# Kernel optimization log

Hardware: AMD Instinct MI355X
Metric: run time of the kernel (lower is better)

The kernel has to match this reference:

```python
import jax, jax.numpy as jnp
import numpy as np

STRIDE = 1
PADDING = (1, 1, 1, 1)  # (left, right, top, bottom), as in torch F.pad for last two dims
NEG_INF = -jnp.inf


def maxplus_conv2d(x, kernel, stride=STRIDE):
    """Tropical (max-plus) conv2d, groups=1.
    x: [B, C, H, W] (already padded), kernel: [O, C, kh, kw].
    out[b,o,h,w] = max_{c,ki,kj} x[b,c,h*s+ki,w*s+kj] + kernel[o,c,ki,kj]
    """
    B, C, H, W = x.shape
    O, Cg, kh, kw = kernel.shape
    Ho = (H - kh) // stride + 1
    Wo = (W - kw) // stride + 1
    out = jnp.full((B, O, Ho, Wo), NEG_INF, dtype=x.dtype)
    # Loop over the small, fixed kernel taps (kh*kw = 9); reductions over the
    # channel axis stay fully vectorized and fuse into a single add+reduce-max.
    for ki in range(kh):
        for kj in range(kw):
            xs = x[:, :, ki:ki + Ho * stride:stride, kj:kj + Wo * stride:stride]  # [B,C,Ho,Wo]
            cand = jnp.max(xs[:, None, :, :, :] + kernel[None, :, :, ki, kj][:, :, :, None, None], axis=2)
            out = jnp.maximum(out, cand)
    return out


def setup_inputs() -> dict:
    key = jax.random.key(0)
    kx, kk = jax.random.split(key)
    x = jax.random.normal(kx, (8, 64, 64, 64), dtype=jnp.float32)
    kernel = jax.random.normal(kk, (64, 64, 3, 3), dtype=jnp.float32) * 0.1
    return {"x": x, "kernel": kernel}


def reference(x, kernel):
    left, right, top, bottom = PADDING
    # MaxPlus semifield: pad with the additive identity of max, i.e. -inf
    xp = jnp.pad(x, ((0, 0), (0, 0), (top, bottom), (left, right)), mode="constant", constant_values=NEG_INF)
    return maxplus_conv2d(xp, kernel, STRIDE)
```

## Files before the change

### kernel.cpp

```cpp
#include <hip/hip_runtime.h>

typedef float v2f __attribute__((ext_vector_type(2)));

#define NEG_INF (-__builtin_huge_valf())

#define CCH   4
#define HB    4
#define ROWS  (HB + 2)
#define XSTR  64
#define SLOTS 6

__device__ __forceinline__ float dpp_shr1(float v, float old) {
    return __int_as_float(__builtin_amdgcn_update_dpp(
        __float_as_int(old), __float_as_int(v), 0x111, 0xF, 0xF, false));
}
__device__ __forceinline__ float dpp_shl1(float v, float old) {
    return __int_as_float(__builtin_amdgcn_update_dpp(
        __float_as_int(old), __float_as_int(v), 0x101, 0xF, 0xF, false));
}

__global__ __launch_bounds__(64, 4)
void maxplus_conv2d_kernel(const float* __restrict__ x,
                           const float* __restrict__ kern,
                           float* __restrict__ out) {
    __shared__ float xs[CCH * ROWS * XSTR];

    const int tid = threadIdx.x;
    const int wg  = tid & 15;
    const int hr  = tid >> 4;
    const int w0  = wg << 2;

    const int h_base = blockIdx.x * HB;
    const int b      = blockIdx.y;
    const int o_base = blockIdx.z << 1;

    const float* xb = x + (size_t)b * 64 * 64 * 64;
    const float* gsrc[SLOTS];
    float*       xdst[SLOTS];
    bool         vmask[SLOTS];
#pragma unroll
    for (int k = 0; k < SLOTS; ++k) {
        int rowid = k * 4 + hr;
        int cl    = rowid / ROWS;
        int r     = rowid - cl * ROWS;
        int gh    = h_base + r - 1;
        bool valid = (unsigned)gh < 64u;
        int  ghc   = valid ? gh : 0;
        gsrc[k]  = xb + ((size_t)cl * 64 + ghc) * 64 + wg * 4;
        xdst[k]  = &xs[rowid * XSTR + wg * 4];
        vmask[k] = valid;
    }

    const float ninf = NEG_INF;

    float acc[2][4];
#pragma unroll
    for (int oo = 0; oo < 2; ++oo)
#pragma unroll
        for (int wi = 0; wi < 4; ++wi)
            acc[oo][wi] = NEG_INF;

    float4 R[SLOTS];
#pragma unroll
    for (int k = 0; k < SLOTS; ++k) R[k] = *(const float4*)gsrc[k];

#pragma unroll 1
    for (int cc = 0; cc < 64; cc += CCH) {
        __syncthreads();

#pragma unroll
        for (int k = 0; k < SLOTS; ++k) {
            float4 v = R[k];
            if (!vmask[k]) v = make_float4(NEG_INF, NEG_INF, NEG_INF, NEG_INF);
            *(float4*)xdst[k] = v;
        }

        __syncthreads();

        if (cc + CCH < 64) {
#pragma unroll
            for (int k = 0; k < SLOTS; ++k) {
                gsrc[k] += CCH * 64 * 64;
                R[k] = *(const float4*)gsrc[k];
            }
        }

        float kv[CCH][2][9];
#pragma unroll
        for (int cl = 0; cl < CCH; ++cl)
#pragma unroll
            for (int oo = 0; oo < 2; ++oo) {
                const float* kp = kern + ((size_t)(o_base + oo) * 64 + (cc + cl)) * 9;
#pragma unroll
                for (int t = 0; t < 9; ++t) kv[cl][oo][t] = kp[t];
            }

#pragma unroll
        for (int cl = 0; cl < CCH; ++cl) {
#pragma unroll
            for (int r = 0; r < 3; ++r) {
                const int rowid = cl * ROWS + hr + r;
                float4 m = *(const float4*)(&xs[rowid * XSTR + w0]);
                float le = dpp_shr1(m.w, ninf);
                float re = dpp_shl1(m.x, ninf);

                v2f P0 = {le,  m.x};
                v2f P1 = {m.y, m.z};
                v2f P2 = {m.w, re };
                v2f Q0 = {m.x, m.y};
                v2f Q1 = {m.z, m.w};

#pragma unroll
                for (int oo = 0; oo < 2; ++oo) {
                    const float* k9 = kv[cl][oo];
                    v2f ka = {k9[3*r+0], k9[3*r+0]};
                    v2f kb = {k9[3*r+1], k9[3*r+1]};
                    v2f kc = {k9[3*r+2], k9[3*r+2]};
                    v2f a0 = P0 + ka, b0 = P1 + ka;
                    v2f a1 = Q0 + kb, b1 = Q1 + kb;
                    v2f a2 = P1 + kc, b2 = P2 + kc;

                    acc[oo][0] = fmaxf(acc[oo][0], fmaxf(fmaxf(a0.x, a1.x), a2.x));
                    acc[oo][1] = fmaxf(acc[oo][1], fmaxf(fmaxf(a0.y, a1.y), a2.y));
                    acc[oo][2] = fmaxf(acc[oo][2], fmaxf(fmaxf(b0.x, b1.x), b2.x));
                    acc[oo][3] = fmaxf(acc[oo][3], fmaxf(fmaxf(b0.y, b1.y), b2.y));
                }
            }
        }
    }

    const int h = h_base + hr;
#pragma unroll
    for (int oo = 0; oo < 2; ++oo) {
        float4 v = make_float4(acc[oo][0], acc[oo][1], acc[oo][2], acc[oo][3]);
        *(float4*)(out + ((((size_t)b * 64 + (o_base + oo)) * 64 + h) * 64 + w0)) = v;
    }
}

extern "C" void kernel_launch(void* const* d_in, const int* in_sizes, int n_in,
                              void* d_out, int out_size, void* d_ws, size_t ws_size,
                              hipStream_t stream) {
    const float* x    = (const float*)d_in[0];
    const float* kern = (const float*)d_in[1];
    float* out = (float*)d_out;

    dim3 grid(16, 8, 32);
    dim3 block(64);
    maxplus_conv2d_kernel<<<grid, block, 0, stream>>>(x, kern, out);
}
```

Baseline: 110.6 us.

## Split channel reduction across two blocks, drop LDS staging, add max-merge pass

Removes the shared-memory staging and barriers. Each thread now loads its three input rows straight from global memory with register double-buffering of the next channel's rows and weights, and out-of-range rows point at a constant -inf row. When workspace is large enough, the 64-channel reduction is split into two halves across twice as many blocks, writing partial maxima to the output and the workspace. A second small kernel then merges the two with elementwise max. This adds parallelism and removes sync overhead, at the cost of an extra launch, extra global traffic, and less cross-thread reuse of input rows.

```diff
diff --git a/kernel.cpp b/kernel.cpp
--- a/kernel.cpp
+++ b/kernel.cpp
@@ -1,14 +1,12 @@
 #include <hip/hip_runtime.h>
-
-typedef float v2f __attribute__((ext_vector_type(2)));
 
 #define NEG_INF (-__builtin_huge_valf())
 
-#define CCH   4
-#define HB    4
-#define ROWS  (HB + 2)
-#define XSTR  64
-#define SLOTS 6
+#define N8 NEG_INF,NEG_INF,NEG_INF,NEG_INF,NEG_INF,NEG_INF,NEG_INF,NEG_INF
+__constant__ __align__(16) float NINF_ROW[64] = {N8,N8,N8,N8,N8,N8,N8,N8};
+#undef N8
+
+typedef float v2f __attribute__((ext_vector_type(2)));
 
 __device__ __forceinline__ float dpp_shr1(float v, float old) {
     return __int_as_float(__builtin_amdgcn_update_dpp(
@@ -22,33 +20,30 @@
 __global__ __launch_bounds__(64, 4)
 void maxplus_conv2d_kernel(const float* __restrict__ x,
                            const float* __restrict__ kern,
-                           float* __restrict__ out) {
-    __shared__ float xs[CCH * ROWS * XSTR];
-
+                           float* __restrict__ out0,
+                           float* __restrict__ out1,
+                           int c_count) {
     const int tid = threadIdx.x;
     const int wg  = tid & 15;
     const int hr  = tid >> 4;
     const int w0  = wg << 2;
 
-    const int h_base = blockIdx.x * HB;
+    const int h      = blockIdx.x * 4 + hr;
     const int b      = blockIdx.y;
-    const int o_base = blockIdx.z << 1;
+    const int half   = blockIdx.z >> 5;
+    const int o_base = (blockIdx.z & 31) << 1;
+    const int c0     = half * c_count;
+    float* dst       = half ? out1 : out0;
 
-    const float* xb = x + (size_t)b * 64 * 64 * 64;
-    const float* gsrc[SLOTS];
-    float*       xdst[SLOTS];
-    bool         vmask[SLOTS];
+    const float* xb = x + (size_t)b * 64 * 64 * 64 + (size_t)c0 * 64 * 64;
+    const float* p[3];
+    int strd[3];
 #pragma unroll
-    for (int k = 0; k < SLOTS; ++k) {
-        int rowid = k * 4 + hr;
-        int cl    = rowid / ROWS;
-        int r     = rowid - cl * ROWS;
-        int gh    = h_base + r - 1;
+    for (int r = 0; r < 3; ++r) {
+        int gh = h - 1 + r;
         bool valid = (unsigned)gh < 64u;
-        int  ghc   = valid ? gh : 0;
-        gsrc[k]  = xb + ((size_t)cl * 64 + ghc) * 64 + wg * 4;
-        xdst[k]  = &xs[rowid * XSTR + wg * 4];
-        vmask[k] = valid;
+        p[r]    = valid ? (xb + (size_t)gh * 64 + w0) : (NINF_ROW + w0);
+        strd[r] = valid ? 4096 : 0;
     }
 
     const float ninf = NEG_INF;
@@ -60,80 +55,89 @@
         for (int wi = 0; wi < 4; ++wi)
             acc[oo][wi] = NEG_INF;
 
-    float4 R[SLOTS];
+    float4 Aq[3], Bq[3];
+    float kvA[2][9], kvB[2][9];
 #pragma unroll
-    for (int k = 0; k < SLOTS; ++k) R[k] = *(const float4*)gsrc[k];
+    for (int r = 0; r < 3; ++r) Aq[r] = *(const float4*)p[r];
+#pragma unroll
+    for (int oo = 0; oo < 2; ++oo) {
+        const float* kp = kern + ((size_t)(o_base + oo) * 64 + c0) * 9;
+#pragma unroll
+        for (int t = 0; t < 9; ++t) kvA[oo][t] = kp[t];
+    }
 
 #pragma unroll 1
-    for (int cc = 0; cc < 64; cc += CCH) {
-        __syncthreads();
-
+    for (int c = 0; c < c_count; ++c) {
+        const bool more = (c + 1 < c_count);
+        if (more) {
 #pragma unroll
-        for (int k = 0; k < SLOTS; ++k) {
-            float4 v = R[k];
-            if (!vmask[k]) v = make_float4(NEG_INF, NEG_INF, NEG_INF, NEG_INF);
-            *(float4*)xdst[k] = v;
-        }
-
-        __syncthreads();
-
-        if (cc + CCH < 64) {
+            for (int r = 0; r < 3; ++r) {
+                p[r] += strd[r];
+                Bq[r] = *(const float4*)p[r];
+            }
 #pragma unroll
-            for (int k = 0; k < SLOTS; ++k) {
-                gsrc[k] += CCH * 64 * 64;
-                R[k] = *(const float4*)gsrc[k];
+            for (int oo = 0; oo < 2; ++oo) {
+                const float* kp = kern + ((size_t)(o_base + oo) * 64 + (c0 + c + 1)) * 9;
+#pragma unroll
+                for (int t = 0; t < 9; ++t) kvB[oo][t] = kp[t];
             }
         }
 
-        float kv[CCH][2][9];
 #pragma unroll
-        for (int cl = 0; cl < CCH; ++cl)
+        for (int r = 0; r < 3; ++r) {
+            float4 m = Aq[r];
+            float le = dpp_shr1(m.w, ninf);
+            float re = dpp_shl1(m.x, ninf);
+
+            v2f P0 = {le,  m.x};
+            v2f P1 = {m.y, m.z};
+            v2f P2 = {m.w, re };
+            v2f Q0 = {m.x, m.y};
+            v2f Q1 = {m.z, m.w};
+
 #pragma unroll
             for (int oo = 0; oo < 2; ++oo) {
-                const float* kp = kern + ((size_t)(o_base + oo) * 64 + (cc + cl)) * 9;
+                const float* k9 = kvA[oo];
+                v2f ka = {k9[3*r+0], k9[3*r+0]};
+                v2f kb = {k9[3*r+1], k9[3*r+1]};
+                v2f kc = {k9[3*r+2], k9[3*r+2]};
+                v2f a0 = P0 + ka, b0 = P1 + ka;
+                v2f a1 = Q0 + kb, b1 = Q1 + kb;
+                v2f a2 = P1 + kc, b2 = P2 + kc;
+
+                acc[oo][0] = fmaxf(acc[oo][0], fmaxf(fmaxf(a0.x, a1.x), a2.x));
+                acc[oo][1] = fmaxf(acc[oo][1], fmaxf(fmaxf(a0.y, a1.y), a2.y));
+                acc[oo][2] = fmaxf(acc[oo][2], fmaxf(fmaxf(b0.x, b1.x), b2.x));
+                acc[oo][3] = fmaxf(acc[oo][3], fmaxf(fmaxf(b0.y, b1.y), b2.y));
+            }
+        }
+
+        if (more) {
 #pragma unroll
-                for (int t = 0; t < 9; ++t) kv[cl][oo][t] = kp[t];
-            }
-
+            for (int r = 0; r < 3; ++r) Aq[r] = Bq[r];
 #pragma unroll
-        for (int cl = 0; cl < CCH; ++cl) {
+            for (int oo = 0; oo < 2; ++oo)
 #pragma unroll
-            for (int r = 0; r < 3; ++r) {
-                const int rowid = cl * ROWS + hr + r;
-                float4 m = *(const float4*)(&xs[rowid * XSTR + w0]);
-                float le = dpp_shr1(m.w, ninf);
-                float re = dpp_shl1(m.x, ninf);
-
-                v2f P0 = {le,  m.x};
-                v2f P1 = {m.y, m.z};
-                v2f P2 = {m.w, re };
-                v2f Q0 = {m.x, m.y};
-                v2f Q1 = {m.z, m.w};
-
-#pragma unroll
-                for (int oo = 0; oo < 2; ++oo) {
-                    const float* k9 = kv[cl][oo];
-                    v2f ka = {k9[3*r+0], k9[3*r+0]};
-                    v2f kb = {k9[3*r+1], k9[3*r+1]};
-                    v2f kc = {k9[3*r+2], k9[3*r+2]};
-                    v2f a0 = P0 + ka, b0 = P1 + ka;
-                    v2f a1 = Q0 + kb, b1 = Q1 + kb;
-                    v2f a2 = P1 + kc, b2 = P2 + kc;
-
-                    acc[oo][0] = fmaxf(acc[oo][0], fmaxf(fmaxf(a0.x, a1.x), a2.x));
-                    acc[oo][1] = fmaxf(acc[oo][1], fmaxf(fmaxf(a0.y, a1.y), a2.y));
-                    acc[oo][2] = fmaxf(acc[oo][2], fmaxf(fmaxf(b0.x, b1.x), b2.x));
-                    acc[oo][3] = fmaxf(acc[oo][3], fmaxf(fmaxf(b0.y, b1.y), b2.y));
-                }
-            }
+                for (int t = 0; t < 9; ++t) kvA[oo][t] = kvB[oo][t];
         }
     }
 
-    const int h = h_base + hr;
 #pragma unroll
     for (int oo = 0; oo < 2; ++oo) {
         float4 v = make_float4(acc[oo][0], acc[oo][1], acc[oo][2], acc[oo][3]);
-        *(float4*)(out + ((((size_t)b * 64 + (o_base + oo)) * 64 + h) * 64 + w0)) = v;
+        *(float4*)(dst + ((((size_t)b * 64 + (o_base + oo)) * 64 + h) * 64 + w0)) = v;
+    }
+}
+
+__global__ __launch_bounds__(256)
+void merge_max_kernel(float* __restrict__ out, const float* __restrict__ ws, int n4) {
+    int i = blockIdx.x * 256 + threadIdx.x;
+    if (i < n4) {
+        float4 a = ((const float4*)out)[i];
+        float4 b = ((const float4*)ws)[i];
+        a.x = fmaxf(a.x, b.x); a.y = fmaxf(a.y, b.y);
+        a.z = fmaxf(a.z, b.z); a.w = fmaxf(a.w, b.w);
+        ((float4*)out)[i] = a;
     }
 }
 
@@ -143,8 +147,16 @@
     const float* x    = (const float*)d_in[0];
     const float* kern = (const float*)d_in[1];
     float* out = (float*)d_out;
+    float* ws  = (float*)d_ws;
 
-    dim3 grid(16, 8, 32);
-    dim3 block(64);
-    maxplus_conv2d_kernel<<<grid, block, 0, stream>>>(x, kern, out);
+    const bool split = ws_size >= (size_t)out_size * sizeof(float);
+    if (split) {
+        dim3 grid(16, 8, 64);
+        maxplus_conv2d_kernel<<<grid, dim3(64), 0, stream>>>(x, kern, out, ws, 32);
+        int n4 = out_size / 4;
+        merge_max_kernel<<<(n4 + 255) / 256, dim3(256), 0, stream>>>(out, ws, n4);
+    } else {
+        dim3 grid(16, 8, 32);
+        maxplus_conv2d_kernel<<<grid, dim3(64), 0, stream>>>(x, kern, out, out, 64);
+    }
 }
```

Result: slower. 132.7 us (+19.9%).

## Double-buffer global prefetch, drop barriers, pad from constant -inf row

Applied to the files above, without the earlier changes.

The kernel now keeps two register buffers of prefetched input rows, so loads for the chunk two steps ahead are in flight while the current chunk computes. The __syncthreads calls are replaced by compiler-only memory fences, on the assumption that the 64-thread block is a single wavefront and LDS operations stay in program order. Out-of-bounds padding rows now read from a constant -inf row with zero stride, which removes the per-store select. The cost is more live registers for the second prefetch buffer, plus reliance on the single-wave ordering assumption for correctness.

```diff
diff --git a/kernel.cpp b/kernel.cpp
--- a/kernel.cpp
+++ b/kernel.cpp
@@ -4,11 +4,16 @@
 
 #define NEG_INF (-__builtin_huge_valf())
 
+#define N8 NEG_INF,NEG_INF,NEG_INF,NEG_INF,NEG_INF,NEG_INF,NEG_INF,NEG_INF
+__constant__ __align__(16) float NINF_ROW[64] = {N8,N8,N8,N8,N8,N8,N8,N8};
+#undef N8
+
 #define CCH   4
-#define HB    4
-#define ROWS  (HB + 2)
+#define ROWS  6
 #define XSTR  64
 #define SLOTS 6
+
+#define CFENCE() asm volatile("" ::: "memory")
 
 __device__ __forceinline__ float dpp_shr1(float v, float old) {
     return __int_as_float(__builtin_amdgcn_update_dpp(
@@ -30,14 +35,14 @@
     const int hr  = tid >> 4;
     const int w0  = wg << 2;
 
-    const int h_base = blockIdx.x * HB;
+    const int h_base = blockIdx.x * 4;
     const int b      = blockIdx.y;
     const int o_base = blockIdx.z << 1;
 
     const float* xb = x + (size_t)b * 64 * 64 * 64;
     const float* gsrc[SLOTS];
     float*       xdst[SLOTS];
-    bool         vmask[SLOTS];
+    int          gstr[SLOTS];
 #pragma unroll
     for (int k = 0; k < SLOTS; ++k) {
         int rowid = k * 4 + hr;
@@ -45,10 +50,10 @@
         int r     = rowid - cl * ROWS;
         int gh    = h_base + r - 1;
         bool valid = (unsigned)gh < 64u;
-        int  ghc   = valid ? gh : 0;
-        gsrc[k]  = xb + ((size_t)cl * 64 + ghc) * 64 + wg * 4;
+        gsrc[k]  = valid ? (xb + ((size_t)cl * 64 + gh) * 64 + wg * 4)
+                         : (NINF_ROW + wg * 4);
+        gstr[k]  = valid ? CCH * 64 * 64 : 0;
         xdst[k]  = &xs[rowid * XSTR + wg * 4];
-        vmask[k] = valid;
     }
 
     const float ninf = NEG_INF;
@@ -60,37 +65,22 @@
         for (int wi = 0; wi < 4; ++wi)
             acc[oo][wi] = NEG_INF;
 
-    float4 R[SLOTS];
+    float4 R0[SLOTS], R1[SLOTS];
 #pragma unroll
-    for (int k = 0; k < SLOTS; ++k) R[k] = *(const float4*)gsrc[k];
+    for (int k = 0; k < SLOTS; ++k) R0[k] = *(const float4*)gsrc[k];
+#pragma unroll
+    for (int k = 0; k < SLOTS; ++k) {
+        gsrc[k] += gstr[k];
+        R1[k] = *(const float4*)gsrc[k];
+    }
 
-#pragma unroll 1
-    for (int cc = 0; cc < 64; cc += CCH) {
-        __syncthreads();
-
-#pragma unroll
-        for (int k = 0; k < SLOTS; ++k) {
-            float4 v = R[k];
-            if (!vmask[k]) v = make_float4(NEG_INF, NEG_INF, NEG_INF, NEG_INF);
-            *(float4*)xdst[k] = v;
-        }
-
-        __syncthreads();
-
-        if (cc + CCH < 64) {
-#pragma unroll
-            for (int k = 0; k < SLOTS; ++k) {
-                gsrc[k] += CCH * 64 * 64;
-                R[k] = *(const float4*)gsrc[k];
-            }
-        }
-
+    auto compute_chunk = [&](int c0) {
         float kv[CCH][2][9];
 #pragma unroll
         for (int cl = 0; cl < CCH; ++cl)
 #pragma unroll
             for (int oo = 0; oo < 2; ++oo) {
-                const float* kp = kern + ((size_t)(o_base + oo) * 64 + (cc + cl)) * 9;
+                const float* kp = kern + ((size_t)(o_base + oo) * 64 + (c0 + cl)) * 9;
 #pragma unroll
                 for (int t = 0; t < 9; ++t) kv[cl][oo][t] = kp[t];
             }
@@ -127,6 +117,35 @@
                 }
             }
         }
+    };
+
+#pragma unroll 1
+    for (int cc = 0; cc < 64; cc += 2 * CCH) {
+        CFENCE();
+#pragma unroll
+        for (int k = 0; k < SLOTS; ++k) *(float4*)xdst[k] = R0[k];
+        CFENCE();
+        if (cc + 8 < 64) {
+#pragma unroll
+            for (int k = 0; k < SLOTS; ++k) {
+                gsrc[k] += gstr[k];
+                R0[k] = *(const float4*)gsrc[k];
+            }
+        }
+        compute_chunk(cc);
+
+        CFENCE();
+#pragma unroll
+        for (int k = 0; k < SLOTS; ++k) *(float4*)xdst[k] = R1[k];
+        CFENCE();
+        if (cc + 12 < 64) {
+#pragma unroll
+            for (int k = 0; k < SLOTS; ++k) {
+                gsrc[k] += gstr[k];
+                R1[k] = *(const float4*)gsrc[k];
+            }
+        }
+        compute_chunk(cc + 4);
     }
 
     const int h = h_base + hr;
```

New measurement: 269.5 us. 2.44x slower.
